# Kernel optimization log

Measured on AMD Instinct MI355X. Metric: run time of the kernel, lower is better.

## Reference

```python
import jax, jax.numpy as jnp
import numpy as np

B, T, D = 2, 2048, 2048
H, KV = 16, 4
HD = D // H            # 128
REP = H // KV          # 4 query heads per kv head


def setup_inputs() -> dict:
    key = jax.random.key(0)
    ks = jax.random.split(key, 5)
    scale = D ** -0.5
    x = jax.random.normal(ks[0], (B, T, D), dtype=jnp.float32)
    Wq = jax.random.normal(ks[1], (D, H * HD), dtype=jnp.float32) * scale
    Wk = jax.random.normal(ks[2], (D, KV * HD), dtype=jnp.float32) * scale
    Wv = jax.random.normal(ks[3], (D, KV * HD), dtype=jnp.float32) * scale
    Wo = jax.random.normal(ks[4], (H * HD, D), dtype=jnp.float32) * scale
    return {"x": x, "Wq": Wq, "Wk": Wk, "Wv": Wv, "Wo": Wo}


def reference(x, Wq, Wk, Wv, Wo):
    b, t, d = x.shape
    # projections; group query heads by their kv head (repeat_interleave order:
    # q head h uses kv head h // REP, i.e. heads are contiguous per group)
    q = (x @ Wq).reshape(b, t, KV, REP, HD)          # bt(g r)d -> b t g r d
    k = (x @ Wk).reshape(b, t, KV, HD)
    v = (x @ Wv).reshape(b, t, KV, HD)
    # scores: [B, KV, REP, T, T] -- equivalent to repeat_interleave of kv heads
    scores = jnp.einsum('btgrd,bsgd->bgrts', q, k) * (HD ** -0.5)
    causal = jnp.tril(jnp.ones((t, t), dtype=bool))
    scores = jnp.where(causal, scores, -jnp.inf)
    weights = jax.nn.softmax(scores, axis=-1)
    out = jnp.einsum('bgrts,bsgd->btgrd', weights, v).reshape(b, t, H * HD)
    return jnp.round(out @ Wo, decimals=4)
```

## Files before the change

### kernel.cpp

```cpp
#include <hip/hip_runtime.h>
#include <hip/hip_bf16.h>
#include <math.h>

#define B_ 2
#define T_ 2048
#define D_ 2048
#define H_ 16
#define KV_ 4
#define HD_ 128
#define REP_ 4
#define QKVSTR 3072

typedef __attribute__((ext_vector_type(8))) short s16x8;
typedef __attribute__((ext_vector_type(4))) short s16x4;
typedef __attribute__((ext_vector_type(4))) float f32x4;
typedef __hip_bfloat16 bf16;

__device__ __forceinline__ short f2bf(float x) {
    bf16 h = __float2bfloat16(x);
    return *reinterpret_cast<short*>(&h);
}

__device__ __forceinline__ void gl2lds16(const void* g, void* l) {
    __builtin_amdgcn_global_load_lds(
        (const __attribute__((address_space(1))) char*)g,
        (__attribute__((address_space(3))) char*)l, 16, 0, 0);
}

__global__ __launch_bounds__(256) void prep(const float* __restrict__ x,
                                            const float* __restrict__ Wq,
                                            const float* __restrict__ Wk,
                                            const float* __restrict__ Wv,
                                            const float* __restrict__ Wo,
                                            bf16* __restrict__ xb,
                                            bf16* __restrict__ Wqkvt,
                                            bf16* __restrict__ Wot,
                                            float qscale) {
    const int bid = blockIdx.x;
    const int t = threadIdx.x;
    if (bid < 4096) {
        int i = (bid * 256 + t) * 8;
        float4 a = *(const float4*)(x + i);
        float4 b = *(const float4*)(x + i + 4);
        short o[8] = {f2bf(a.x), f2bf(a.y), f2bf(a.z), f2bf(a.w),
                      f2bf(b.x), f2bf(b.y), f2bf(b.z), f2bf(b.w)};
        *(s16x8*)(xb + i) = *(const s16x8*)o;
        return;
    }
    __shared__ short tile[64 * 72];
    const float* W; bf16* dst; int N; float scale; int seg;
    if (bid < 5120)      { seg = bid - 4096; W = Wq; dst = Wqkvt;                      N = 2048; scale = qscale; }
    else if (bid < 5376) { seg = bid - 5120; W = Wk; dst = Wqkvt + (size_t)2048 * D_;  N = 512;  scale = 1.f; }
    else if (bid < 5632) { seg = bid - 5376; W = Wv; dst = Wqkvt + (size_t)2560 * D_;  N = 512;  scale = 1.f; }
    else                 { seg = bid - 5632; W = Wo; dst = Wot;                        N = 2048; scale = 1.f; }
    const int k0 = (seg & 31) * 64, n0 = (seg >> 5) * 64;
    const int r = t >> 2, c0 = (t & 3) * 16;
    const float* src = W + (size_t)(k0 + r) * N + n0 + c0;
    #pragma unroll
    for (int i = 0; i < 16; i += 4) {
        float4 v = *(const float4*)(src + i);
        tile[r * 72 + c0 + i + 0] = f2bf(v.x * scale);
        tile[r * 72 + c0 + i + 1] = f2bf(v.y * scale);
        tile[r * 72 + c0 + i + 2] = f2bf(v.z * scale);
        tile[r * 72 + c0 + i + 3] = f2bf(v.w * scale);
    }
    __syncthreads();
    short tmp[16];
    #pragma unroll
    for (int i = 0; i < 16; ++i) tmp[i] = tile[(c0 + i) * 72 + r];
    bf16* d = dst + (size_t)(n0 + r) * D_ + k0 + c0;
    *(s16x8*)(d)     = *(const s16x8*)&tmp[0];
    *(s16x8*)(d + 8) = *(const s16x8*)&tmp[8];
}

template<typename OUTT, int ROUND, int WVT>
__global__ __launch_bounds__(256, 3) void gemm_nt(const bf16* __restrict__ A,
                                                  const bf16* __restrict__ Bt,
                                                  OUTT* __restrict__ C,
                                                  bf16* __restrict__ Vtg,
                                                  int M, int N, int K) {
    __shared__ short As[128 * 64];
    __shared__ short Bs[128 * 64];
    const int tid = threadIdx.x;
    const int lane = tid & 63;
    const int wave = tid >> 6;
    const int quad = lane >> 4;
    const int l16 = lane & 15;
    const int wr = wave >> 1, wc = wave & 1;
    const int row0 = blockIdx.y * 128;
    const int col0 = blockIdx.x * 128;

    f32x4 acc[4][4] = {};

    for (int k0 = 0; k0 < K; k0 += 64) {
        __syncthreads();
        #pragma unroll
        for (int i = 0; i < 4; ++i) {
            int g = i * 256 + tid;
            int row = g >> 3;
            int cs = (g & 7) ^ (row & 7);
            gl2lds16(A + (size_t)(row0 + row) * K + k0 + cs * 8, &As[g * 8]);
        }
        #pragma unroll
        for (int i = 0; i < 4; ++i) {
            int g = i * 256 + tid;
            int row = g >> 3;
            int cs = (g & 7) ^ (row & 7);
            gl2lds16(Bt + (size_t)(col0 + row) * K + k0 + cs * 8, &Bs[g * 8]);
        }
        __syncthreads();
        #pragma unroll
        for (int kk = 0; kk < 2; ++kk) {
            s16x8 af[4], bfr[4];
            #pragma unroll
            for (int i = 0; i < 4; ++i) {
                int row = wr * 64 + i * 16 + l16;
                int c = (kk * 4 + quad) ^ (row & 7);
                af[i] = *(const s16x8*)&As[row * 64 + c * 8];
            }
            #pragma unroll
            for (int j = 0; j < 4; ++j) {
                int row = wc * 64 + j * 16 + l16;
                int c = (kk * 4 + quad) ^ (row & 7);
                bfr[j] = *(const s16x8*)&Bs[row * 64 + c * 8];
            }
            #pragma unroll
            for (int i = 0; i < 4; ++i)
                #pragma unroll
                for (int j = 0; j < 4; ++j)
                    acc[i][j] = __builtin_amdgcn_mfma_f32_16x16x32_bf16(
                        af[i], bfr[j], acc[i][j], 0, 0, 0);
        }
    }

    #pragma unroll
    for (int i = 0; i < 4; ++i) {
        #pragma unroll
        for (int j = 0; j < 4; ++j) {
            const int col = col0 + wc * 64 + j * 16 + l16;
            const int rowb = row0 + wr * 64 + i * 16 + quad * 4;
            #pragma unroll
            for (int r = 0; r < 4; ++r) {
                float v = acc[i][j][r];
                if (ROUND) v = rintf(v * 1e4f) * 1e-4f;
                if constexpr (sizeof(OUTT) == 2)
                    C[(size_t)(rowb + r) * N + col] = __float2bfloat16(v);
                else
                    C[(size_t)(rowb + r) * N + col] = v;
            }
            if constexpr (WVT) {
                if (col >= 2560) {
                    const int dcol = (col - 2560) & 127;
                    const int g = (col - 2560) >> 7;
                    const int b = rowb >> 11;
                    const int t = rowb & 2047;
                    short pk[4] = {f2bf(acc[i][j][0]), f2bf(acc[i][j][1]),
                                   f2bf(acc[i][j][2]), f2bf(acc[i][j][3])};
                    *(s16x4*)&Vtg[(size_t)((b * KV_ + g) * HD_ + dcol) * T_ + t] =
                        *(const s16x4*)pk;
                }
            }
        }
    }
}

__global__ __launch_bounds__(256, 3) void flash7(const bf16* __restrict__ Q,
                                                 const bf16* __restrict__ K,
                                                 const bf16* __restrict__ Vtg,
                                                 bf16* __restrict__ O) {
    __shared__ short smem[20480];

    const int h = blockIdx.x;
    const int b = blockIdx.y & 1;
    const int qt = 31 - (blockIdx.y >> 1);
    const int g = h >> 2;
    const int tid = threadIdx.x;
    const int lane = tid & 63;
    const int wave = tid >> 6;
    const int quad = lane >> 4;
    const int l16 = lane & 15;
    const int q0g = qt * 64 + wave * 16;

    s16x8 qf[4];
    {
        const bf16* qp = Q + (size_t)(b * T_ + q0g + l16) * QKVSTR + h * HD_ + quad * 8;
        #pragma unroll
        for (int ks = 0; ks < 4; ++ks) qf[ks] = *(const s16x8*)(qp + ks * 32);
    }

    const bf16* Kp = K + (size_t)(b * T_) * QKVSTR + g * HD_;
    const bf16* Vp = Vtg + (size_t)((b * KV_ + g) * HD_) * T_;

    float l_part[4] = {0.f, 0.f, 0.f, 0.f};
    f32x4 oacc[8] = {};

    for (int j = 0; j <= qt; ++j) {
        const int s0 = j * 64;
        __syncthreads();
        #pragma unroll
        for (int i = 0; i < 4; ++i) {
            int g2 = i * 256 + tid;
            int s = g2 >> 4;
            int cs = (g2 & 15) ^ (s & 15);
            gl2lds16(Kp + (size_t)(s0 + s) * QKVSTR + cs * 8, &smem[g2 * 8]);
        }
        #pragma unroll
        for (int i = 0; i < 4; ++i) {
            int g2 = i * 256 + tid;
            int d = g2 >> 3;
            int cs = (g2 & 7) ^ (d & 7);
            gl2lds16(Vp + (size_t)d * T_ + s0 + cs * 8, &smem[8192 + g2 * 8]);
        }
        __syncthreads();

        f32x4 sacc[4] = {};
        #pragma unroll
        for (int ks = 0; ks < 4; ++ks) {
            s16x8 kf[4];
            #pragma unroll
            for (int ct = 0; ct < 4; ++ct) {
                int srow = ct * 16 + l16;
                int c = (ks * 4 + quad) ^ (srow & 15);
                kf[ct] = *(const s16x8*)&smem[srow * 128 + c * 8];
            }
            #pragma unroll
            for (int ct = 0; ct < 4; ++ct)
                sacc[ct] = __builtin_amdgcn_mfma_f32_16x16x32_bf16(
                    qf[ks], kf[ct], sacc[ct], 0, 0, 0);
        }

        const bool diag = (j == qt);
        #pragma unroll
        for (int r = 0; r < 4; ++r) {
            const int qrow = q0g + quad * 4 + r;
            if (diag) {
                #pragma unroll
                for (int ct = 0; ct < 4; ++ct)
                    if (s0 + ct * 16 + l16 > qrow) sacc[ct][r] = -INFINITY;
            }
            float psum = 0.f;
            #pragma unroll
            for (int ct = 0; ct < 4; ++ct) {
                float p = exp2f(sacc[ct][r]);
                sacc[ct][r] = p;
                psum += p;
            }
            l_part[r] += psum;
        }

        #pragma unroll
        for (int ct = 0; ct < 4; ++ct)
            #pragma unroll
            for (int r = 0; r < 4; ++r) {
                int row = wave * 16 + quad * 4 + r;
                int chunk = (ct * 2 + (l16 >> 3)) ^ (row & 7);
                smem[16384 + row * 64 + chunk * 8 + (l16 & 7)] = f2bf(sacc[ct][r]);
            }

        #pragma unroll
        for (int kk = 0; kk < 2; ++kk) {
            int prow = wave * 16 + l16;
            int pc = (kk * 4 + quad) ^ (prow & 7);
            const s16x8 pf = *(const s16x8*)&smem[16384 + prow * 64 + pc * 8];
            #pragma unroll
            for (int dt = 0; dt < 8; ++dt) {
                int d = dt * 16 + l16;
                int c = (kk * 4 + quad) ^ (d & 7);
                const s16x8 vf = *(const s16x8*)&smem[8192 + d * 64 + c * 8];
                oacc[dt] = __builtin_amdgcn_mfma_f32_16x16x32_bf16(
                    vf, pf, oacc[dt], 0, 0, 0);
            }
        }
    }

    #pragma unroll
    for (int r = 0; r < 4; ++r) {
        float x = l_part[r];
        x += __shfl_xor(x, 1);
        x += __shfl_xor(x, 2);
        x += __shfl_xor(x, 4);
        x += __shfl_xor(x, 8);
        l_part[r] = x;
    }
    const int srcl = (l16 >> 2) << 4;
    const float lv0 = __shfl(l_part[0], srcl);
    const float lv1 = __shfl(l_part[1], srcl);
    const float lv2 = __shfl(l_part[2], srcl);
    const float lv3 = __shfl(l_part[3], srcl);
    const int rsel = l16 & 3;
    const float lsel = rsel == 0 ? lv0 : rsel == 1 ? lv1 : rsel == 2 ? lv2 : lv3;
    const float invl = 1.f / lsel;

    __syncthreads();

    #pragma unroll
    for (int dt = 0; dt < 8; ++dt) {
        short tmp[4];
        #pragma unroll
        for (int r = 0; r < 4; ++r) tmp[r] = f2bf(oacc[dt][r] * invl);
        *(long long*)&smem[(wave * 16 + l16) * 136 + dt * 16 + quad * 4] =
            *(const long long*)tmp;
    }
    const int r2 = wave * 16 + (lane >> 2);
    bf16* op = O + (size_t)(b * T_ + qt * 64 + r2) * (H_ * HD_) + h * HD_;
    #pragma unroll
    for (int c = 0; c < 4; ++c) {
        int chunk = c * 4 + (lane & 3);
        *(s16x8*)(op + chunk * 8) = *(const s16x8*)&smem[r2 * 136 + chunk * 8];
    }
}

extern "C" void kernel_launch(void* const* d_in, const int* in_sizes, int n_in,
                              void* d_out, int out_size, void* d_ws, size_t ws_size,
                              hipStream_t stream) {
    const float* x  = (const float*)d_in[0];
    const float* Wq = (const float*)d_in[1];
    const float* Wk = (const float*)d_in[2];
    const float* Wv = (const float*)d_in[3];
    const float* Wo = (const float*)d_in[4];
    float* out = (float*)d_out;

    const size_t NR = (size_t)B_ * T_;
    bf16* ws = (bf16*)d_ws;
    bf16* xb    = ws;
    bf16* Wqkvt = xb + NR * D_;
    bf16* Wot   = Wqkvt + (size_t)QKVSTR * D_;
    bf16* QKVb  = Wot + (size_t)D_ * D_;
    bf16* Vtg   = QKVb + NR * QKVSTR;
    bf16* Ab    = Vtg + (size_t)B_ * KV_ * HD_ * T_;

    const float qscale = 1.4426950408889634f / sqrtf((float)HD_);

    prep<<<6656, 256, 0, stream>>>(x, Wq, Wk, Wv, Wo, xb, Wqkvt, Wot, qscale);

    gemm_nt<bf16, 0, 1><<<dim3(QKVSTR / 128, NR / 128), 256, 0, stream>>>(
        xb, Wqkvt, QKVb, Vtg, (int)NR, QKVSTR, D_);

    flash7<<<dim3(H_, 64), 256, 0, stream>>>(QKVb, QKVb + 2048, Vtg, Ab);

    gemm_nt<float, 1, 0><<<dim3(D_ / 128, NR / 128), 256, 0, stream>>>(
        Ab, Wot, out, nullptr, (int)NR, D_, H_ * HD_);
}
```

Baseline: 276.6 us.

## Rewrite flash attention with 32x32 MFMA and register-resident P tiles

The attention kernel now gives each workgroup 128 query rows, with 32 rows per wave, and uses 32x32x16 bf16 MFMA instead of 16x16x32. The probability tile is packed to bf16 in registers and rearranged with v_permlane32_swap, so it no longer round-trips through LDS, and the LDS P buffer is dropped. Each K/V tile loaded into LDS is shared by twice as many query rows, which cuts global and LDS traffic per query. The costs are half as many workgroups (512), more accumulator registers, waves skipping tiles above the causal diagonal while still taking part in the barriers, and uncoalesced scalar bf16 stores for the output.

```diff
diff --git a/kernel.cpp b/kernel.cpp
--- a/kernel.cpp
+++ b/kernel.cpp
@@ -14,6 +14,7 @@
 typedef __attribute__((ext_vector_type(8))) short s16x8;
 typedef __attribute__((ext_vector_type(4))) short s16x4;
 typedef __attribute__((ext_vector_type(4))) float f32x4;
+typedef __attribute__((ext_vector_type(16))) float f32x16;
 typedef __hip_bfloat16 bf16;
 
 __device__ __forceinline__ short f2bf(float x) {
@@ -164,37 +165,39 @@
     }
 }
 
-__global__ __launch_bounds__(256, 3) void flash7(const bf16* __restrict__ Q,
+__global__ __launch_bounds__(256, 3) void flash8(const bf16* __restrict__ Q,
                                                  const bf16* __restrict__ K,
                                                  const bf16* __restrict__ Vtg,
                                                  bf16* __restrict__ O) {
-    __shared__ short smem[20480];
+    __shared__ short smem[16384];
 
     const int h = blockIdx.x;
     const int b = blockIdx.y & 1;
-    const int qt = 31 - (blockIdx.y >> 1);
+    const int qt = 15 - (blockIdx.y >> 1);
     const int g = h >> 2;
     const int tid = threadIdx.x;
     const int lane = tid & 63;
     const int wave = tid >> 6;
-    const int quad = lane >> 4;
-    const int l16 = lane & 15;
-    const int q0g = qt * 64 + wave * 16;
-
-    s16x8 qf[4];
+    const int l32 = lane & 31;
+    const int hi = lane >> 5;
+    const int qw0 = qt * 128 + wave * 32;
+    const int qg = qw0 + l32;
+
+    s16x8 qf[8];
     {
-        const bf16* qp = Q + (size_t)(b * T_ + q0g + l16) * QKVSTR + h * HD_ + quad * 8;
-        #pragma unroll
-        for (int ks = 0; ks < 4; ++ks) qf[ks] = *(const s16x8*)(qp + ks * 32);
+        const bf16* qp = Q + (size_t)(b * T_ + qg) * QKVSTR + h * HD_ + hi * 8;
+        #pragma unroll
+        for (int kt = 0; kt < 8; ++kt) qf[kt] = *(const s16x8*)(qp + kt * 16);
     }
 
     const bf16* Kp = K + (size_t)(b * T_) * QKVSTR + g * HD_;
     const bf16* Vp = Vtg + (size_t)((b * KV_ + g) * HD_) * T_;
 
-    float l_part[4] = {0.f, 0.f, 0.f, 0.f};
-    f32x4 oacc[8] = {};
-
-    for (int j = 0; j <= qt; ++j) {
+    float l_part = 0.f;
+    f32x16 oacc[4] = {};
+
+    const int jmax = 2 * qt + 1;
+    for (int j = 0; j <= jmax; ++j) {
         const int s0 = j * 64;
         __syncthreads();
         #pragma unroll
@@ -213,100 +216,76 @@
         }
         __syncthreads();
 
-        f32x4 sacc[4] = {};
-        #pragma unroll
-        for (int ks = 0; ks < 4; ++ks) {
-            s16x8 kf[4];
-            #pragma unroll
-            for (int ct = 0; ct < 4; ++ct) {
-                int srow = ct * 16 + l16;
-                int c = (ks * 4 + quad) ^ (srow & 15);
-                kf[ct] = *(const s16x8*)&smem[srow * 128 + c * 8];
-            }
-            #pragma unroll
-            for (int ct = 0; ct < 4; ++ct)
-                sacc[ct] = __builtin_amdgcn_mfma_f32_16x16x32_bf16(
-                    qf[ks], kf[ct], sacc[ct], 0, 0, 0);
-        }
-
-        const bool diag = (j == qt);
-        #pragma unroll
-        for (int r = 0; r < 4; ++r) {
-            const int qrow = q0g + quad * 4 + r;
-            if (diag) {
+        if (s0 >= qw0 + 32) continue;
+
+        f32x16 sacc[2] = {};
+        #pragma unroll
+        for (int kt = 0; kt < 8; ++kt) {
+            #pragma unroll
+            for (int mt = 0; mt < 2; ++mt) {
+                int s = mt * 32 + l32;
+                int c = (kt * 2 + hi) ^ (s & 15);
+                const s16x8 kf = *(const s16x8*)&smem[s * 128 + c * 8];
+                sacc[mt] = __builtin_amdgcn_mfma_f32_32x32x16_bf16(
+                    kf, qf[kt], sacc[mt], 0, 0, 0);
+            }
+        }
+
+        const bool diagw = (s0 + 63 > qw0);
+        #pragma unroll
+        for (int mt = 0; mt < 2; ++mt) {
+            #pragma unroll
+            for (int r = 0; r < 16; ++r) {
+                float sv = sacc[mt][r];
+                if (diagw) {
+                    int sg = s0 + mt * 32 + (r & 3) + 8 * (r >> 2) + 4 * hi;
+                    if (sg > qg) sv = -INFINITY;
+                }
+                float e = exp2f(sv);
+                sacc[mt][r] = e;
+                l_part += e;
+            }
+            #pragma unroll
+            for (int kts = 0; kts < 2; ++kts) {
+                const int o = kts * 8;
+                unsigned w01, w23, w45, w67;
+                asm("v_cvt_pk_bf16_f32 %0, %1, %2"
+                    : "=v"(w01) : "v"(sacc[mt][o + 0]), "v"(sacc[mt][o + 1]));
+                asm("v_cvt_pk_bf16_f32 %0, %1, %2"
+                    : "=v"(w23) : "v"(sacc[mt][o + 2]), "v"(sacc[mt][o + 3]));
+                asm("v_cvt_pk_bf16_f32 %0, %1, %2"
+                    : "=v"(w45) : "v"(sacc[mt][o + 4]), "v"(sacc[mt][o + 5]));
+                asm("v_cvt_pk_bf16_f32 %0, %1, %2"
+                    : "=v"(w67) : "v"(sacc[mt][o + 6]), "v"(sacc[mt][o + 7]));
+                asm("v_permlane32_swap_b32 %0, %1" : "+v"(w01), "+v"(w45));
+                asm("v_permlane32_swap_b32 %0, %1" : "+v"(w23), "+v"(w67));
+                union { unsigned u[4]; s16x8 v; } pu;
+                pu.u[0] = w01; pu.u[1] = w23; pu.u[2] = w45; pu.u[3] = w67;
+                const s16x8 pa = pu.v;
                 #pragma unroll
-                for (int ct = 0; ct < 4; ++ct)
-                    if (s0 + ct * 16 + l16 > qrow) sacc[ct][r] = -INFINITY;
-            }
-            float psum = 0.f;
-            #pragma unroll
-            for (int ct = 0; ct < 4; ++ct) {
-                float p = exp2f(sacc[ct][r]);
-                sacc[ct][r] = p;
-                psum += p;
-            }
-            l_part[r] += psum;
-        }
-
-        #pragma unroll
-        for (int ct = 0; ct < 4; ++ct)
-            #pragma unroll
-            for (int r = 0; r < 4; ++r) {
-                int row = wave * 16 + quad * 4 + r;
-                int chunk = (ct * 2 + (l16 >> 3)) ^ (row & 7);
-                smem[16384 + row * 64 + chunk * 8 + (l16 & 7)] = f2bf(sacc[ct][r]);
-            }
-
-        #pragma unroll
-        for (int kk = 0; kk < 2; ++kk) {
-            int prow = wave * 16 + l16;
-            int pc = (kk * 4 + quad) ^ (prow & 7);
-            const s16x8 pf = *(const s16x8*)&smem[16384 + prow * 64 + pc * 8];
-            #pragma unroll
-            for (int dt = 0; dt < 8; ++dt) {
-                int d = dt * 16 + l16;
-                int c = (kk * 4 + quad) ^ (d & 7);
-                const s16x8 vf = *(const s16x8*)&smem[8192 + d * 64 + c * 8];
-                oacc[dt] = __builtin_amdgcn_mfma_f32_16x16x32_bf16(
-                    vf, pf, oacc[dt], 0, 0, 0);
-            }
-        }
-    }
-
+                for (int nt = 0; nt < 4; ++nt) {
+                    int d = nt * 32 + l32;
+                    int c = ((mt * 2 + kts) * 2 + hi) ^ (d & 7);
+                    const s16x8 vf = *(const s16x8*)&smem[8192 + d * 64 + c * 8];
+                    oacc[nt] = __builtin_amdgcn_mfma_f32_32x32x16_bf16(
+                        pa, vf, oacc[nt], 0, 0, 0);
+                }
+            }
+        }
+    }
+
+    l_part += __shfl_xor(l_part, 32);
+    const float invl = 1.f / l_part;
+
+    bf16* op = O + (size_t)(b * T_ + qw0) * (H_ * HD_) + h * HD_;
     #pragma unroll
-    for (int r = 0; r < 4; ++r) {
-        float x = l_part[r];
-        x += __shfl_xor(x, 1);
-        x += __shfl_xor(x, 2);
-        x += __shfl_xor(x, 4);
-        x += __shfl_xor(x, 8);
-        l_part[r] = x;
-    }
-    const int srcl = (l16 >> 2) << 4;
-    const float lv0 = __shfl(l_part[0], srcl);
-    const float lv1 = __shfl(l_part[1], srcl);
-    const float lv2 = __shfl(l_part[2], srcl);
-    const float lv3 = __shfl(l_part[3], srcl);
-    const int rsel = l16 & 3;
-    const float lsel = rsel == 0 ? lv0 : rsel == 1 ? lv1 : rsel == 2 ? lv2 : lv3;
-    const float invl = 1.f / lsel;
-
-    __syncthreads();
-
-    #pragma unroll
-    for (int dt = 0; dt < 8; ++dt) {
-        short tmp[4];
-        #pragma unroll
-        for (int r = 0; r < 4; ++r) tmp[r] = f2bf(oacc[dt][r] * invl);
-        *(long long*)&smem[(wave * 16 + l16) * 136 + dt * 16 + quad * 4] =
-            *(const long long*)tmp;
-    }
-    const int r2 = wave * 16 + (lane >> 2);
-    bf16* op = O + (size_t)(b * T_ + qt * 64 + r2) * (H_ * HD_) + h * HD_;
-    #pragma unroll
-    for (int c = 0; c < 4; ++c) {
-        int chunk = c * 4 + (lane & 3);
-        *(s16x8*)(op + chunk * 8) = *(const s16x8*)&smem[r2 * 136 + chunk * 8];
+    for (int r = 0; r < 16; ++r) {
+        const int qrow = (r & 3) + 8 * (r >> 2) + 4 * hi;
+        const float il = __shfl(invl, qrow);
+        #pragma unroll
+        for (int nt = 0; nt < 4; ++nt)
+            op[(size_t)qrow * (H_ * HD_) + nt * 32 + l32] =
+                __float2bfloat16(oacc[nt][r] * il);
     }
 }
 
@@ -336,7 +315,7 @@
     gemm_nt<bf16, 0, 1><<<dim3(QKVSTR / 128, NR / 128), 256, 0, stream>>>(
         xb, Wqkvt, QKVb, Vtg, (int)NR, QKVSTR, D_);
 
-    flash7<<<dim3(H_, 64), 256, 0, stream>>>(QKVb, QKVb + 2048, Vtg, Ab);
+    flash8<<<dim3(H_, 32), 256, 0, stream>>>(QKVb, QKVb + 2048, Vtg, Ab);
 
     gemm_nt<float, 1, 0><<<dim3(D_ / 128, NR / 128), 256, 0, stream>>>(
         Ab, Wot, out, nullptr, (int)NR, D_, H_ * HD_);
```

Measured after the change: 325.2 us. 17.6% more time.
